# Performance work log

Measured on AMD Instinct MI355X. Metric: run time of the kernel, lower is better.

Reference implementation:

```python
import math
import jax, jax.numpy as jnp
import numpy as np

B, S, D, H, V, NZ = 2, 2048, 1024, 16, 4096, 10
DK = D // H
KAPPA = 1.0
GAMMA_VALS = [14.1347, 21.022, 25.0109, 30.4249, 32.9351,
              37.5862, 40.9187, 43.3271, 48.0052, 49.7738]


def setup_inputs() -> dict:
    key = jax.random.key(0)
    ks = jax.random.split(key, 12)
    w_scale = 1.0 / math.sqrt(D)
    x = jax.random.normal(ks[0], (B, S, D), dtype=jnp.float32)
    wq = jax.random.normal(ks[1], (D, D), dtype=jnp.float32) * w_scale
    wk = jax.random.normal(ks[2], (D, D), dtype=jnp.float32) * w_scale
    wv = jax.random.normal(ks[3], (D, D), dtype=jnp.float32) * w_scale
    wo = jax.random.normal(ks[4], (D, D), dtype=jnp.float32) * w_scale
    bq = jax.random.normal(ks[5], (D,), dtype=jnp.float32) * 0.01
    bk = jax.random.normal(ks[6], (D,), dtype=jnp.float32) * 0.01
    bv = jax.random.normal(ks[7], (D,), dtype=jnp.float32) * 0.01
    bo = jax.random.normal(ks[8], (D,), dtype=jnp.float32) * 0.01
    semantic_token_ids = jax.random.randint(ks[9], (B, S), 0, V)
    # constitutional charter mask: mostly-allowed boolean (stored as float buffer)
    omega_mask = (jax.random.uniform(ks[10], (V, V)) < 0.95).astype(jnp.float32)
    causal_mask = jnp.tril(jnp.ones((S, S), dtype=bool))
    gamma = jnp.asarray(GAMMA_VALS[:NZ], dtype=jnp.float32)
    return {
        "x": x, "wq": wq, "bq": bq, "wk": wk, "bk": bk,
        "wv": wv, "bv": bv, "wo": wo, "bo": bo,
        "omega_mask": omega_mask, "gamma": gamma,
        "semantic_token_ids": semantic_token_ids, "causal_mask": causal_mask,
    }


def _memory_kernel(seq_len, gamma):
    idx = jnp.arange(seq_len, dtype=jnp.float32)
    delta = jnp.abs(idx[:, None] - idx[None, :])            # [S, S]
    decay = jnp.exp(-KAPPA * delta)
    log_delta = jnp.log(delta + 1.0)
    cos_sum = jnp.sum(jnp.cos(gamma[:, None, None] * log_delta[None]), axis=0)
    return decay * cos_sum                                   # [S, S]


def reference(x, wq, bq, wk, bk, wv, bv, wo, bo,
              omega_mask, gamma, semantic_token_ids, causal_mask):
    batch, seq_len, _ = x.shape
    q = (x @ wq.T + bq).reshape(batch, seq_len, H, DK)
    k = (x @ wk.T + bk).reshape(batch, seq_len, H, DK)
    v = (x @ wv.T + bv).reshape(batch, seq_len, H, DK)
    scores = jnp.einsum('bihd,bjhd->bhij', q, k) / math.sqrt(DK)  # [B,H,S,S]
    M = _memory_kernel(seq_len, gamma)                            # [S,S]
    scores = scores * M[None, None]
    # seq_omega[b,i,j] = omega_mask[ids[b,i], ids[b,j]]
    ids = semantic_token_ids
    seq_omega = omega_mask[ids[:, :, None], ids[:, None, :]]      # [B,S,S]
    scores = jnp.where(seq_omega[:, None] == 0, -1e9, scores)
    scores = jnp.where(causal_mask[None, None], scores, -1e9)
    attn = jax.nn.softmax(scores, axis=-1)
    out = jnp.einsum('bhij,bjhd->bihd', attn, v).reshape(batch, seq_len, D)
    return out @ wo.T + bo
```

## Files before the change

### kernel.cpp

```cpp
#include <hip/hip_runtime.h>
#include <math.h>
#include <float.h>

#define B_ 2
#define S_ 2048
#define D_ 1024
#define H_ 16
#define V_ 4096
#define NZ_ 10
#define BS_ (B_ * S_)

typedef __attribute__((ext_vector_type(8))) __bf16 bf16x8;
typedef __attribute__((ext_vector_type(4))) float f32x4;

#define MFMA16(a, b, c) __builtin_amdgcn_mfma_f32_16x16x32_bf16((a), (b), (c), 0, 0, 0)

__device__ __forceinline__ unsigned short f2bf(float f) {
  unsigned u = __builtin_bit_cast(unsigned, f);
  u = (u + 0x7FFFu + ((u >> 16) & 1u)) >> 16;
  return (unsigned short)u;
}
__device__ __forceinline__ float bf2f(unsigned short h) {
  unsigned u = ((unsigned)h) << 16;
  return __builtin_bit_cast(float, u);
}

__global__ __launch_bounds__(256) void prep_kernel(
    const float* __restrict__ x,
    const float* __restrict__ wq, const float* __restrict__ wk,
    const float* __restrict__ wv, const float* __restrict__ wo,
    const float* __restrict__ omega, const float* __restrict__ gamma,
    unsigned short* __restrict__ xh, unsigned short* __restrict__ xl,
    unsigned short* __restrict__ wqh, unsigned short* __restrict__ wql,
    unsigned short* __restrict__ wkh, unsigned short* __restrict__ wkl,
    unsigned short* __restrict__ wvh, unsigned short* __restrict__ woh,
    unsigned long long* __restrict__ obit, float* __restrict__ mbg) {
  const int bid = blockIdx.x;
  const int t = threadIdx.x;
  if (bid < 4096) {
    int i = (bid * 256 + t) * 4;
    float4 v = *(const float4*)(x + i);
    ushort4 h;
    h.x = f2bf(v.x); h.y = f2bf(v.y); h.z = f2bf(v.z); h.w = f2bf(v.w);
    *(ushort4*)(xh + i) = h;
    ushort4 l;
    l.x = f2bf(v.x - bf2f(h.x));
    l.y = f2bf(v.y - bf2f(h.y));
    l.z = f2bf(v.z - bf2f(h.z));
    l.w = f2bf(v.w - bf2f(h.w));
    *(ushort4*)(xl + i) = l;
  } else if (bid < 8192) {
    int idx = ((bid - 4096) * 256 + t) * 4;
    int w = idx >> 20;
    int off = idx & ((1 << 20) - 1);
    const float* src; unsigned short* hi; unsigned short* lo;
    if (w == 0)      { src = wq; hi = wqh; lo = wql; }
    else if (w == 1) { src = wk; hi = wkh; lo = wkl; }
    else if (w == 2) { src = wv; hi = wvh; lo = nullptr; }
    else             { src = wo; hi = woh; lo = nullptr; }
    float4 v = *(const float4*)(src + off);
    ushort4 h;
    h.x = f2bf(v.x); h.y = f2bf(v.y); h.z = f2bf(v.z); h.w = f2bf(v.w);
    *(ushort4*)(hi + off) = h;
    if (lo) {
      ushort4 l;
      l.x = f2bf(v.x - bf2f(h.x));
      l.y = f2bf(v.y - bf2f(h.y));
      l.z = f2bf(v.z - bf2f(h.z));
      l.w = f2bf(v.w - bf2f(h.w));
      *(ushort4*)(lo + off) = l;
    }
  } else if (bid < 8192 + 65536) {
    int e = (bid - 8192) * 256 + t;
    bool ok = omega[e] != 0.f;
    unsigned long long mask = __ballot(ok);
    if ((t & 63) == 0) obit[e >> 6] = mask;
  } else {
    if (t < 64) {
      float delta = (float)t;
      float ld = logf(delta + 1.f);
      float cs = 0.f;
#pragma unroll
      for (int z = 0; z < NZ_; ++z) cs += cosf(gamma[z] * ld);
      mbg[t] = expf(-delta) * cs * 0.125f;
    }
  }
}

template <int NT>
__device__ __forceinline__ void stage_tiles(const unsigned short* const* gb,
                                            int wave, int lane, int K, int k0,
                                            unsigned short* dst) {
#pragma unroll
  for (int tile = 0; tile < NT; ++tile) {
#pragma unroll
    for (int half = 0; half < 2; ++half) {
      int c = wave + half * 4;
      int s = (c << 6) + lane;
      int row = s >> 2;
      int cq = (s & 3) ^ ((s >> 3) & 3);
      const unsigned short* g = gb[tile] + (size_t)row * K + k0 + (cq << 3);
      unsigned short* l = dst + tile * 4096 + (s << 3);
      __builtin_amdgcn_global_load_lds((const __attribute__((address_space(1))) void*)g,
                                       (__attribute__((address_space(3))) void*)l,
                                       16, 0, 0);
    }
  }
}

__device__ __forceinline__ void frag_loads(const unsigned short* tb, int base, int wsel,
                                           int m, int quad, bf16x8 (&f)[4]) {
#pragma unroll
  for (int i = 0; i < 4; ++i) {
    int r = wsel * 64 + i * 16 + m;
    f[i] = *(const bf16x8*)&tb[base + r * 32 + ((quad ^ ((r >> 1) & 3)) << 3)];
  }
}

__device__ __forceinline__ void qkv_compute(const unsigned short* tb, bool split,
                                            int wm, int wn, int m, int quad,
                                            f32x4 (&acc)[4][4]) {
  bf16x8 afh[4], bfh[4];
  frag_loads(tb, 0 * 4096, wm, m, quad, afh);
  frag_loads(tb, 1 * 4096, wn, m, quad, bfh);
  if (split) {
    bf16x8 afl[4], bfl[4];
    frag_loads(tb, 2 * 4096, wm, m, quad, afl);
    frag_loads(tb, 3 * 4096, wn, m, quad, bfl);
#pragma unroll
    for (int mt = 0; mt < 4; ++mt)
#pragma unroll
      for (int nt = 0; nt < 4; ++nt) {
        acc[mt][nt] = MFMA16(afh[mt], bfh[nt], acc[mt][nt]);
        acc[mt][nt] = MFMA16(afl[mt], bfh[nt], acc[mt][nt]);
        acc[mt][nt] = MFMA16(afh[mt], bfl[nt], acc[mt][nt]);
      }
  } else {
#pragma unroll
    for (int mt = 0; mt < 4; ++mt)
#pragma unroll
      for (int nt = 0; nt < 4; ++nt)
        acc[mt][nt] = MFMA16(afh[mt], bfh[nt], acc[mt][nt]);
  }
}

__global__ __launch_bounds__(256) void mfma_gemm_qkv(
    const unsigned short* __restrict__ xh, const unsigned short* __restrict__ xl,
    const unsigned short* __restrict__ wqh, const unsigned short* __restrict__ wql,
    const unsigned short* __restrict__ wkh, const unsigned short* __restrict__ wkl,
    const unsigned short* __restrict__ wvh,
    const float* __restrict__ bq, const float* __restrict__ bk,
    const float* __restrict__ bv,
    unsigned short* __restrict__ qoh, unsigned short* __restrict__ qol,
    unsigned short* __restrict__ koh, unsigned short* __restrict__ kol,
    unsigned short* __restrict__ voh) {
  __shared__ unsigned short tiles[2][4 * 4096];
  const int t = threadIdx.x;
  const int wave = t >> 6, lane = t & 63;
  const int which = blockIdx.x >> 3;
  const int n0 = (blockIdx.x & 7) * 128;
  const int i0 = blockIdx.y * 128;
  const int K = D_, N = D_;
  const int wm = wave >> 1, wn = wave & 1;
  const int m = lane & 15, quad = lane >> 4;

  const unsigned short* Wh = (which == 0) ? wqh : (which == 1) ? wkh : wvh;
  const unsigned short* Wl = (which == 0) ? wql : wkl;
  const float* bias = (which == 0) ? bq : (which == 1) ? bk : bv;
  unsigned short* Chi = (which == 0) ? qoh : (which == 1) ? koh : voh;
  unsigned short* Clo = (which == 0) ? qol : (which == 1) ? kol : nullptr;
  const bool split = (which < 2);

  const unsigned short* gb[4];
  gb[0] = xh + (size_t)i0 * K;
  gb[1] = Wh + (size_t)n0 * K;
  gb[2] = xl + (size_t)i0 * K;
  gb[3] = Wl + (size_t)n0 * K;

  f32x4 acc[4][4] = {};

  if (split) stage_tiles<4>(gb, wave, lane, K, 0, tiles[0]);
  else       stage_tiles<2>(gb, wave, lane, K, 0, tiles[0]);
  __syncthreads();

  for (int k0 = 0; k0 < K; k0 += 64) {
    if (split) stage_tiles<4>(gb, wave, lane, K, k0 + 32, tiles[1]);
    else       stage_tiles<2>(gb, wave, lane, K, k0 + 32, tiles[1]);
    qkv_compute(tiles[0], split, wm, wn, m, quad, acc);
    __syncthreads();
    if (k0 + 64 < K) {
      if (split) stage_tiles<4>(gb, wave, lane, K, k0 + 64, tiles[0]);
      else       stage_tiles<2>(gb, wave, lane, K, k0 + 64, tiles[0]);
    }
    qkv_compute(tiles[1], split, wm, wn, m, quad, acc);
    __syncthreads();
  }

  float bvv[4];
#pragma unroll
  for (int nt = 0; nt < 4; ++nt) bvv[nt] = bias[n0 + wn * 64 + nt * 16 + m];
#pragma unroll
  for (int mt = 0; mt < 4; ++mt) {
    int rbase = i0 + wm * 64 + mt * 16 + quad * 4;
#pragma unroll
    for (int nt = 0; nt < 4; ++nt) {
      int col = n0 + wn * 64 + nt * 16 + m;
#pragma unroll
      for (int r = 0; r < 4; ++r) {
        float val = acc[mt][nt][r] + bvv[nt];
        size_t idx = (size_t)(rbase + r) * N + col;
        unsigned short hv = f2bf(val);
        Chi[idx] = hv;
        if (Clo) Clo[idx] = f2bf(val - bf2f(hv));
      }
    }
  }
}

__global__ __launch_bounds__(256) void mfma_gemm_o(const unsigned short* __restrict__ Ah,
                                                   const unsigned short* __restrict__ Wh,
                                                   const float* __restrict__ bias,
                                                   float* __restrict__ C,
                                                   int M, int N, int K) {
  __shared__ unsigned short tiles[2][2 * 4096];
  const int t = threadIdx.x;
  const int wave = t >> 6, lane = t & 63;
  const int i0 = blockIdx.y * 128, n0 = blockIdx.x * 128;
  const int wm = wave >> 1, wn = wave & 1;
  const int m = lane & 15, quad = lane >> 4;

  const unsigned short* gb[2];
  gb[0] = Ah + (size_t)i0 * K;
  gb[1] = Wh + (size_t)n0 * K;

  f32x4 acc[4][4] = {};

  stage_tiles<2>(gb, wave, lane, K, 0, tiles[0]);
  __syncthreads();

  for (int k0 = 0; k0 < K; k0 += 64) {
    stage_tiles<2>(gb, wave, lane, K, k0 + 32, tiles[1]);
    qkv_compute(tiles[0], false, wm, wn, m, quad, acc);
    __syncthreads();
    if (k0 + 64 < K) stage_tiles<2>(gb, wave, lane, K, k0 + 64, tiles[0]);
    qkv_compute(tiles[1], false, wm, wn, m, quad, acc);
    __syncthreads();
  }

  float bvv[4];
#pragma unroll
  for (int nt = 0; nt < 4; ++nt) bvv[nt] = bias[n0 + wn * 64 + nt * 16 + m];
#pragma unroll
  for (int mt = 0; mt < 4; ++mt) {
    int rbase = i0 + wm * 64 + mt * 16 + quad * 4;
#pragma unroll
    for (int nt = 0; nt < 4; ++nt) {
      int col = n0 + wn * 64 + nt * 16 + m;
#pragma unroll
      for (int r = 0; r < 4; ++r)
        C[(size_t)(rbase + r) * N + col] = acc[mt][nt][r] + bvv[nt];
    }
  }
}

__global__ void ts8_kernel(const unsigned short* __restrict__ vh, float* __restrict__ ts8) {
  int idx = blockIdx.x * 256 + threadIdx.x;
  int d = idx % D_;
  int bg = idx / D_;
  int g = bg % 256;
  int b = bg / 256;
  const unsigned short* p = vh + (size_t)(b * S_ + g * 8) * D_ + d;
  float s = 0.f;
#pragma unroll
  for (int j = 0; j < 8; ++j) s += bf2f(p[(size_t)j * D_]);
  ts8[idx] = s;
}

__global__ __launch_bounds__(256) void tsp_kernel(const float* __restrict__ ts8,
                                                  float* __restrict__ tsp) {
  int b = blockIdx.x >> 2;
  int d = ((blockIdx.x & 3) << 8) + threadIdx.x;
  float s = 0.f;
  tsp[((size_t)b * 33 + 0) * D_ + d] = 0.f;
  for (int u = 0; u < 256; ++u) {
    s += ts8[((size_t)b * 256 + u) * D_ + d];
    if ((u & 7) == 7) tsp[((size_t)b * 33 + (u >> 3) + 1) * D_ + d] = s;
  }
}

__global__ __launch_bounds__(256) void farsum_kernel(const unsigned short* __restrict__ vh,
                                                     const float* __restrict__ ts8,
                                                     const float* __restrict__ tsp,
                                                     const int* __restrict__ ids,
                                                     const unsigned long long* __restrict__ obit,
                                                     unsigned short* __restrict__ farsum,
                                                     int* __restrict__ c0,
                                                     unsigned long long* __restrict__ bm) {
  const int b = blockIdx.x / S_;
  const int i = blockIdx.x % S_;
  const int t = threadIdx.x;
  const int idi = ids[b * S_ + i];
  const unsigned long long* orow = obit + ((size_t)idi << 6);

  if (t < 64) {
    int jj = i - t;
    bool ok = false;
    if (jj >= 0) {
      int idj = ids[b * S_ + jj];
      ok = (orow[idj >> 6] >> (idj & 63)) & 1ull;
    }
    unsigned long long mask = __ballot(ok);
    if (t == 0) bm[blockIdx.x] = mask;
  }

  if (i < 64) {
    if (t == 0) c0[blockIdx.x] = 0;
    return;
  }
  const int jmax = i - 64;
  const int F = jmax + 1;
  const int d0 = t * 4;
  const int T = F >> 6;
  const int G8 = (F & 63) >> 3;

  float4 acc = *(const float4*)(tsp + ((size_t)b * 33 + T) * D_ + d0);
  for (int u = 0; u < G8; ++u) {
    float4 x = *(const float4*)(ts8 + ((size_t)b * 256 + T * 8 + u) * D_ + d0);
    acc.x += x.x; acc.y += x.y; acc.z += x.z; acc.w += x.w;
  }
  for (int j = (T << 6) + (G8 << 3); j <= jmax; ++j) {
    ushort4 x = *(const ushort4*)(vh + ((size_t)(b * S_) + j) * D_ + d0);
    acc.x += bf2f(x.x); acc.y += bf2f(x.y);
    acc.z += bf2f(x.z); acc.w += bf2f(x.w);
  }

  __shared__ int list[256];
  __shared__ int cnt;
  int nmask = 0;
  for (int base = 0; base < F; base += 256) {
    if (t == 0) cnt = 0;
    __syncthreads();
    int j = base + t;
    if (j <= jmax) {
      int idj = ids[b * S_ + j];
      if (!((orow[idj >> 6] >> (idj & 63)) & 1ull)) list[atomicAdd(&cnt, 1)] = j;
    }
    __syncthreads();
    int c = cnt;
    nmask += c;
    for (int mm = 0; mm < c; ++mm) {
      int jm = list[mm];
      ushort4 x = *(const ushort4*)(vh + ((size_t)(b * S_) + jm) * D_ + d0);
      acc.x -= bf2f(x.x); acc.y -= bf2f(x.y);
      acc.z -= bf2f(x.z); acc.w -= bf2f(x.w);
    }
    __syncthreads();
  }
  ushort4 o;
  o.x = f2bf(acc.x); o.y = f2bf(acc.y); o.z = f2bf(acc.z); o.w = f2bf(acc.w);
  *(ushort4*)(farsum + (size_t)(b * S_ + i) * D_ + d0) = o;
  if (t == 0) c0[blockIdx.x] = F - nmask;
}

__global__ __launch_bounds__(256, 3) void attn4_kernel(
    const unsigned short* __restrict__ qh, const unsigned short* __restrict__ ql,
    const unsigned short* __restrict__ kh, const unsigned short* __restrict__ kl,
    const unsigned short* __restrict__ vh, const unsigned short* __restrict__ farsum,
    const int* __restrict__ c0arr, const float* __restrict__ tsp,
    const unsigned long long* __restrict__ bm, const float* __restrict__ mbg,
    unsigned short* __restrict__ out) {
  const int h = blockIdx.x, i0 = blockIdx.y * 64, b = blockIdx.z;
  const int jt0 = i0 - 64;
  __shared__ unsigned short Qhs[64 * 72];
  __shared__ unsigned short Khs[128 * 72];
  __shared__ unsigned short Vt[64 * 136];
  __shared__ float mrow[64], lrow[64], Mband[64];
  __shared__ float rmaxw[4][32], rsumw[4][32];
  __shared__ unsigned long long bmr[64];
  __shared__ int c0r[64];
  const int t = threadIdx.x, lane = t & 63, wave = t >> 6;
  const int m = lane & 15, quad = lane >> 4;
  const int wm = wave >> 1, wn = wave & 1;

  bf16x8 aL[2][2], bL[4][2];
#pragma unroll
  for (int mt = 0; mt < 2; ++mt)
#pragma unroll
    for (int kc = 0; kc < 2; ++kc) {
      int row = i0 + wm * 32 + mt * 16 + m;
      aL[mt][kc] = *(const bf16x8*)(ql + ((size_t)(b * S_) + row) * D_ + h * 64 + kc * 32 + quad * 8);
    }
#pragma unroll
  for (int nt = 0; nt < 4; ++nt)
#pragma unroll
    for (int kc = 0; kc < 2; ++kc) {
      int jr = jt0 + wn * 64 + nt * 16 + m;
      if (jr < 0) jr = 0;
      bL[nt][kc] = *(const bf16x8*)(kl + ((size_t)(b * S_) + jr) * D_ + h * 64 + kc * 32 + quad * 8);
    }

  for (int c = t; c < 1024; c += 256) {
    int r = c >> 4, d4 = (c & 15) << 2;
    size_t g = ((size_t)(b * S_) + i0 + r) * D_ + h * 64 + d4;
    *(ushort4*)&Qhs[r * 72 + d4] = *(const ushort4*)(qh + g);
  }
  for (int c = t; c < 2048; c += 256) {
    int r = c >> 4, d4 = (c & 15) << 2;
    int jr = jt0 + r;
    if (jr < 0) jr = 0;
    size_t g = ((size_t)(b * S_) + jr) * D_ + h * 64 + d4;
    *(ushort4*)&Khs[r * 72 + d4] = *(const ushort4*)(kh + g);
    ushort4 vv = *(const ushort4*)(vh + g);
    Vt[(d4 + 0) * 136 + r] = vv.x; Vt[(d4 + 1) * 136 + r] = vv.y;
    Vt[(d4 + 2) * 136 + r] = vv.z; Vt[(d4 + 3) * 136 + r] = vv.w;
  }
  if (t < 64) {
    Mband[t] = mbg[t];
    int grow = b * S_ + i0 + t;
    bmr[t] = bm[grow];
    int c0v = c0arr[grow];
    c0r[t] = c0v;
    mrow[t] = (c0v > 0) ? 0.f : -FLT_MAX;
  }
  __syncthreads();

  f32x4 accS[2][4] = {};
#pragma unroll
  for (int kc = 0; kc < 2; ++kc) {
    bf16x8 aH[2], bH[4];
#pragma unroll
    for (int mt = 0; mt < 2; ++mt)
      aH[mt] = *(const bf16x8*)&Qhs[(wm * 32 + mt * 16 + m) * 72 + kc * 32 + quad * 8];
#pragma unroll
    for (int nt = 0; nt < 4; ++nt)
      bH[nt] = *(const bf16x8*)&Khs[(wn * 64 + nt * 16 + m) * 72 + kc * 32 + quad * 8];
#pragma unroll
    for (int mt = 0; mt < 2; ++mt)
#pragma unroll
      for (int nt = 0; nt < 4; ++nt) {
        accS[mt][nt] = MFMA16(aH[mt], bH[nt], accS[mt][nt]);
        accS[mt][nt] = MFMA16(aL[mt][kc], bH[nt], accS[mt][nt]);
        accS[mt][nt] = MFMA16(aH[mt], bL[nt][kc], accS[mt][nt]);
      }
  }

  float rmx[2][4];
#pragma unroll
  for (int mt = 0; mt < 2; ++mt)
#pragma unroll
    for (int r = 0; r < 4; ++r) rmx[mt][r] = -FLT_MAX;
#pragma unroll
  for (int mt = 0; mt < 2; ++mt)
#pragma unroll
    for (int nt = 0; nt < 4; ++nt)
#pragma unroll
      for (int r = 0; r < 4; ++r) {
        int il = wm * 32 + mt * 16 + quad * 4 + r;
        int jl = wn * 64 + nt * 16 + m;
        int dlt = il + 64 - jl;
        float s = -FLT_MAX;
        if (dlt >= 0 && dlt < 64 && ((bmr[il] >> dlt) & 1ull))
          s = accS[mt][nt][r] * Mband[dlt];
        accS[mt][nt][r] = s;
        rmx[mt][r] = fmaxf(rmx[mt][r], s);
      }
#pragma unroll
  for (int off = 1; off < 16; off <<= 1)
#pragma unroll
    for (int mt = 0; mt < 2; ++mt)
#pragma unroll
      for (int r = 0; r < 4; ++r)
        rmx[mt][r] = fmaxf(rmx[mt][r], __shfl_xor(rmx[mt][r], off));
  if (m == 0)
#pragma unroll
    for (int mt = 0; mt < 2; ++mt)
#pragma unroll
      for (int r = 0; r < 4; ++r)
        rmaxw[wave][mt * 16 + quad * 4 + r] = rmx[mt][r];
  __syncthreads();
  if (t < 64) {
    int wmw = t >> 5, idx = t & 31;
    float tmax = fmaxf(rmaxw[wmw * 2][idx], rmaxw[wmw * 2 + 1][idx]);
    mrow[t] = fmaxf(mrow[t], tmax);
  }
  __syncthreads();

  unsigned short* Pl = Khs;
  float rs[2][4] = {};
#pragma unroll
  for (int mt = 0; mt < 2; ++mt)
#pragma unroll
    for (int nt = 0; nt < 4; ++nt)
#pragma unroll
      for (int r = 0; r < 4; ++r) {
        int il = wm * 32 + mt * 16 + quad * 4 + r;
        int jl = wn * 64 + nt * 16 + m;
        float s = accS[mt][nt][r];
        float p = (s > -1e37f) ? expf(s - mrow[il]) : 0.f;
        rs[mt][r] += p;
        Pl[il * 136 + jl] = f2bf(p);
      }
#pragma unroll
  for (int off = 1; off < 16; off <<= 1)
#pragma unroll
    for (int mt = 0; mt < 2; ++mt)
#pragma unroll
      for (int r = 0; r < 4; ++r)
        rs[mt][r] += __shfl_xor(rs[mt][r], off);
  if (m == 0)
#pragma unroll
    for (int mt = 0; mt < 2; ++mt)
#pragma unroll
      for (int r = 0; r < 4; ++r)
        rsumw[wave][mt * 16 + quad * 4 + r] = rs[mt][r];
  __syncthreads();
  if (t < 64) {
    int wmw = t >> 5, idx = t & 31;
    lrow[t] = rsumw[wmw * 2][idx] + rsumw[wmw * 2 + 1][idx];
  }

  f32x4 accO[2][2] = {};
#pragma unroll
  for (int kc = 0; kc < 4; ++kc) {
    bf16x8 aP[2], bV[2];
#pragma unroll
    for (int mt = 0; mt < 2; ++mt)
      aP[mt] = *(const bf16x8*)&Pl[(wm * 32 + mt * 16 + m) * 136 + kc * 32 + quad * 8];
#pragma unroll
    for (int nt = 0; nt < 2; ++nt)
      bV[nt] = *(const bf16x8*)&Vt[(wn * 32 + nt * 16 + m) * 136 + kc * 32 + quad * 8];
#pragma unroll
    for (int mt = 0; mt < 2; ++mt)
#pragma unroll
      for (int nt = 0; nt < 2; ++nt)
        accO[mt][nt] = MFMA16(aP[mt], bV[nt], accO[mt][nt]);
  }
  __syncthreads();

#pragma unroll
  for (int mt = 0; mt < 2; ++mt)
#pragma unroll
    for (int r = 0; r < 4; ++r) {
      int il = wm * 32 + mt * 16 + quad * 4 + r;
      int gi = i0 + il;
      float mv = mrow[il], l = lrow[il];
      int C0 = c0r[il];
      float efar = (C0 > 0) ? expf(-mv) : 0.f;
      float denom = l + (float)C0 * efar;
      bool degen = (l == 0.f && C0 == 0);
      if (degen) denom = (float)S_;
      float inv = 1.f / denom;
#pragma unroll
      for (int nt = 0; nt < 2; ++nt) {
        int d = wn * 32 + nt * 16 + m;
        size_t base = ((size_t)(b * S_) + gi) * D_ + h * 64 + d;
        float o = accO[mt][nt][r];
        if (C0 > 0) o += efar * bf2f(farsum[base]);
        if (degen) o = tsp[((size_t)b * 33 + 32) * D_ + h * 64 + d];
        out[base] = f2bf(o * inv);
      }
    }
}

extern "C" void kernel_launch(void* const* d_in, const int* in_sizes, int n_in,
                              void* d_out, int out_size, void* d_ws, size_t ws_size,
                              hipStream_t stream) {
  const float* x     = (const float*)d_in[0];
  const float* wq    = (const float*)d_in[1];
  const float* bq    = (const float*)d_in[2];
  const float* wk    = (const float*)d_in[3];
  const float* bk    = (const float*)d_in[4];
  const float* wv    = (const float*)d_in[5];
  const float* bv    = (const float*)d_in[6];
  const float* wo    = (const float*)d_in[7];
  const float* bo    = (const float*)d_in[8];
  const float* omega = (const float*)d_in[9];
  const float* gamma = (const float*)d_in[10];
  const int*   ids   = (const int*)d_in[11];
  float* out = (float*)d_out;

  char* ws = (char*)d_ws;
  const size_t SZH = (size_t)BS_ * D_ * 2;
  const size_t WH  = (size_t)D_ * D_ * 2;
  unsigned short* qhb = (unsigned short*)(ws);
  unsigned short* qlb = (unsigned short*)(ws + 1 * SZH);
  unsigned short* khb = (unsigned short*)(ws + 2 * SZH);
  unsigned short* klb = (unsigned short*)(ws + 3 * SZH);
  unsigned short* vhb = (unsigned short*)(ws + 4 * SZH);
  unsigned short* xl    = (unsigned short*)(ws + 5 * SZH);
  unsigned short* fsumh = xl;
  unsigned short* xh    = (unsigned short*)(ws + 6 * SZH);
  unsigned short* ah    = xh;
  char* wp = ws + 7 * SZH;
  unsigned short* wqh = (unsigned short*)(wp);
  unsigned short* wql = (unsigned short*)(wp + 1 * WH);
  unsigned short* wkh = (unsigned short*)(wp + 2 * WH);
  unsigned short* wkl = (unsigned short*)(wp + 3 * WH);
  unsigned short* wvh = (unsigned short*)(wp + 4 * WH);
  unsigned short* woh = (unsigned short*)(wp + 5 * WH);
  char* tail = wp + 6 * WH;
  unsigned long long* obit = (unsigned long long*)tail;
  float* ts8  = (float*)(tail + (size_t)V_ * 64 * 8);
  float* ts64 = (float*)((char*)ts8 + (size_t)B_ * 256 * D_ * 4);
  float* tsp  = (float*)((char*)ts64 + (size_t)B_ * 32 * D_ * 4);
  int* c0 = (int*)((char*)tsp + (size_t)B_ * 33 * D_ * 4);
  unsigned long long* bmask = (unsigned long long*)((char*)c0 + (size_t)BS_ * 4);
  float* mbg = (float*)((char*)bmask + (size_t)BS_ * 8);

  prep_kernel<<<8192 + 65536 + 1, 256, 0, stream>>>(
      x, wq, wk, wv, wo, omega, gamma,
      xh, xl, wqh, wql, wkh, wkl, wvh, woh, obit, mbg);

  mfma_gemm_qkv<<<dim3(24, 32), 256, 0, stream>>>(xh, xl, wqh, wql, wkh, wkl, wvh,
                                                  bq, bk, bv, qhb, qlb, khb, klb, vhb);

  ts8_kernel<<<(B_ * 256 * D_) / 256, 256, 0, stream>>>(vhb, ts8);
  tsp_kernel<<<B_ * 4, 256, 0, stream>>>(ts8, tsp);
  farsum_kernel<<<B_ * S_, 256, 0, stream>>>(vhb, ts8, tsp, ids, obit, fsumh, c0, bmask);
  attn4_kernel<<<dim3(H_, S_ / 64, B_), 256, 0, stream>>>(qhb, qlb, khb, klb, vhb, fsumh, c0,
                                                          tsp, bmask, mbg, ah);

  mfma_gemm_o<<<dim3(D_ / 128, BS_ / 128), 256, 0, stream>>>(ah, woh, bo, out, BS_, D_, D_);
}
```

Measured before the change: 400.4 us.

## Parallelize prefix sums and replace shared-list masking with per-wave ballot iteration

The serial tsp prefix kernel, which ran on only 8 blocks and looped 256 times per thread, is replaced by two wide kernels: one reduces groups of eight ts8 rows into ts64, and one computes each prefix entry directly. In farsum, the shared-memory list built with atomics and guarded by three barriers per 256-column chunk is replaced by a wave-level ballot over 64 columns, iterating set bits with ctz. This removes block syncs and LDS atomics, at the cost of an extra launch and some redundant prefix work. Each wave now walks its own masked bits, and the result is unchanged because every wave covers the full range.

Result: no change. 398.2 us (-0.5%).

```diff
diff --git a/kernel.cpp b/kernel.cpp
--- a/kernel.cpp
+++ b/kernel.cpp
@@ -276,16 +276,27 @@
   ts8[idx] = s;
 }
 
-__global__ __launch_bounds__(256) void tsp_kernel(const float* __restrict__ ts8,
-                                                  float* __restrict__ tsp) {
-  int b = blockIdx.x >> 2;
-  int d = ((blockIdx.x & 3) << 8) + threadIdx.x;
+__global__ void ts64_kernel(const float* __restrict__ ts8, float* __restrict__ ts64) {
+  int idx = blockIdx.x * 256 + threadIdx.x;
+  int d = idx % D_;
+  int bT = idx / D_;
+  int T = bT % 32;
+  int b = bT / 32;
   float s = 0.f;
-  tsp[((size_t)b * 33 + 0) * D_ + d] = 0.f;
-  for (int u = 0; u < 256; ++u) {
-    s += ts8[((size_t)b * 256 + u) * D_ + d];
-    if ((u & 7) == 7) tsp[((size_t)b * 33 + (u >> 3) + 1) * D_ + d] = s;
-  }
+#pragma unroll
+  for (int u = 0; u < 8; ++u) s += ts8[((size_t)b * 256 + T * 8 + u) * D_ + d];
+  ts64[idx] = s;
+}
+
+__global__ void tsp2_kernel(const float* __restrict__ ts64, float* __restrict__ tsp) {
+  int idx = blockIdx.x * 256 + threadIdx.x;
+  int d = idx % D_;
+  int bT = idx / D_;
+  int T = bT % 33;
+  int b = bT / 33;
+  float s = 0.f;
+  for (int u = 0; u < T; ++u) s += ts64[((size_t)b * 32 + u) * D_ + d];
+  tsp[idx] = s;
 }
 
 __global__ __launch_bounds__(256) void farsum_kernel(const unsigned short* __restrict__ vh,
@@ -299,6 +310,7 @@
   const int b = blockIdx.x / S_;
   const int i = blockIdx.x % S_;
   const int t = threadIdx.x;
+  const int lane = t & 63;
   const int idi = ids[b * S_ + i];
   const unsigned long long* orow = obit + ((size_t)idi << 6);
 
@@ -334,28 +346,26 @@
     acc.z += bf2f(x.z); acc.w += bf2f(x.w);
   }
 
-  __shared__ int list[256];
-  __shared__ int cnt;
   int nmask = 0;
-  for (int base = 0; base < F; base += 256) {
-    if (t == 0) cnt = 0;
-    __syncthreads();
-    int j = base + t;
+  for (int base = 0; base < F; base += 64) {
+    int j = base + lane;
+    bool masked = false;
     if (j <= jmax) {
       int idj = ids[b * S_ + j];
-      if (!((orow[idj >> 6] >> (idj & 63)) & 1ull)) list[atomicAdd(&cnt, 1)] = j;
-    }
-    __syncthreads();
-    int c = cnt;
-    nmask += c;
-    for (int mm = 0; mm < c; ++mm) {
-      int jm = list[mm];
+      masked = !((orow[idj >> 6] >> (idj & 63)) & 1ull);
+    }
+    unsigned long long mk = __ballot(masked);
+    nmask += (int)__popcll(mk);
+    while (mk) {
+      int p = (int)__builtin_ctzll(mk);
+      mk &= mk - 1;
+      int jm = base + p;
       ushort4 x = *(const ushort4*)(vh + ((size_t)(b * S_) + jm) * D_ + d0);
       acc.x -= bf2f(x.x); acc.y -= bf2f(x.y);
       acc.z -= bf2f(x.z); acc.w -= bf2f(x.w);
     }
-    __syncthreads();
-  }
+  }
+
   ushort4 o;
   o.x = f2bf(acc.x); o.y = f2bf(acc.y); o.z = f2bf(acc.z); o.w = f2bf(acc.w);
   *(ushort4*)(farsum + (size_t)(b * S_ + i) * D_ + d0) = o;
@@ -615,7 +625,8 @@
                                                   bq, bk, bv, qhb, qlb, khb, klb, vhb);
 
   ts8_kernel<<<(B_ * 256 * D_) / 256, 256, 0, stream>>>(vhb, ts8);
-  tsp_kernel<<<B_ * 4, 256, 0, stream>>>(ts8, tsp);
+  ts64_kernel<<<(B_ * 32 * D_) / 256, 256, 0, stream>>>(ts8, ts64);
+  tsp2_kernel<<<(B_ * 33 * D_) / 256, 256, 0, stream>>>(ts64, tsp);
   farsum_kernel<<<B_ * S_, 256, 0, stream>>>(vhb, ts8, tsp, ids, obit, fsumh, c0, bmask);
   attn4_kernel<<<dim3(H_, S_ / 64, B_), 256, 0, stream>>>(qhb, qlb, khb, klb, vhb, fsumh, c0,
                                                           tsp, bmask, mbg, ah);
```

## Compute far-field masked V sums as a bitmask MFMA GEMM over transposed V

Applied to the files above, without the earlier changes.

The far-field sum of allowed V rows is now computed as a GEMM between a 0/1 mask matrix, expanded from per-row bitmasks into bf16, and a transposed V stored as [B,D,S]. The old per-row prefix-sum-minus-masked-list loop is removed. A new maskbits kernel builds the bitmasks and counts, and the QKV GEMM writes V transposed through LDS. The attention kernel also stages the K low part in LDS and loads V from the transposed layout. Blocks in the triangular GEMM are paired long with short for balance, but the GEMM does more raw FLOPs than the sparse subtraction approach.

After: 361.2 us. 1.11x faster.

```diff
diff --git a/kernel.cpp b/kernel.cpp
--- a/kernel.cpp
+++ b/kernel.cpp
@@ -12,6 +12,7 @@
 
 typedef __attribute__((ext_vector_type(8))) __bf16 bf16x8;
 typedef __attribute__((ext_vector_type(4))) float f32x4;
+typedef unsigned long long ull;
 
 #define MFMA16(a, b, c) __builtin_amdgcn_mfma_f32_16x16x32_bf16((a), (b), (c), 0, 0, 0)
 
@@ -34,7 +35,7 @@
     unsigned short* __restrict__ wqh, unsigned short* __restrict__ wql,
     unsigned short* __restrict__ wkh, unsigned short* __restrict__ wkl,
     unsigned short* __restrict__ wvh, unsigned short* __restrict__ woh,
-    unsigned long long* __restrict__ obit, float* __restrict__ mbg) {
+    ull* __restrict__ obit, float* __restrict__ mbg) {
   const int bid = blockIdx.x;
   const int t = threadIdx.x;
   if (bid < 4096) {
@@ -73,7 +74,7 @@
   } else if (bid < 8192 + 65536) {
     int e = (bid - 8192) * 256 + t;
     bool ok = omega[e] != 0.f;
-    unsigned long long mask = __ballot(ok);
+    ull mask = __ballot(ok);
     if ((t & 63) == 0) obit[e >> 6] = mask;
   } else {
     if (t < 64) {
@@ -85,6 +86,50 @@
       mbg[t] = expf(-delta) * cs * 0.125f;
     }
   }
+}
+
+__global__ __launch_bounds__(256) void maskbits_kernel(const int* __restrict__ ids,
+                                                       const ull* __restrict__ obit,
+                                                       ull* __restrict__ fmask,
+                                                       int* __restrict__ c0,
+                                                       ull* __restrict__ bm) {
+  const int grow = blockIdx.x;
+  const int b = grow >> 11, i = grow & 2047;
+  const int t = threadIdx.x, lane = t & 63, wave = t >> 6;
+  const int idi = ids[grow];
+  const ull* orow = obit + ((size_t)idi << 6);
+  __shared__ int cnt;
+  if (t == 0) cnt = 0;
+  if (t < 64) {
+    int jj = i - t;
+    bool ok = false;
+    if (jj >= 0) {
+      int idj = ids[b * S_ + jj];
+      ok = (orow[idj >> 6] >> (idj & 63)) & 1ull;
+    }
+    ull mask = __ballot(ok);
+    if (t == 0) bm[grow] = mask;
+  }
+  __syncthreads();
+  const int jmax = i - 64;
+  int pc = 0;
+#pragma unroll
+  for (int c = 0; c < 8; ++c) {
+    int j = c * 256 + t;
+    bool on = false;
+    if (j <= jmax) {
+      int idj = ids[b * S_ + j];
+      on = (orow[idj >> 6] >> (idj & 63)) & 1ull;
+    }
+    ull mk = __ballot(on);
+    if (lane == 0) {
+      fmask[(size_t)grow * 32 + c * 4 + wave] = mk;
+      pc += (int)__popcll(mk);
+    }
+  }
+  if (lane == 0 && pc) atomicAdd(&cnt, pc);
+  __syncthreads();
+  if (t == 0) c0[grow] = cnt;
 }
 
 template <int NT>
@@ -153,7 +198,7 @@
     const float* __restrict__ bv,
     unsigned short* __restrict__ qoh, unsigned short* __restrict__ qol,
     unsigned short* __restrict__ koh, unsigned short* __restrict__ kol,
-    unsigned short* __restrict__ voh) {
+    unsigned short* __restrict__ vt) {
   __shared__ unsigned short tiles[2][4 * 4096];
   const int t = threadIdx.x;
   const int wave = t >> 6, lane = t & 63;
@@ -167,7 +212,7 @@
   const unsigned short* Wh = (which == 0) ? wqh : (which == 1) ? wkh : wvh;
   const unsigned short* Wl = (which == 0) ? wql : wkl;
   const float* bias = (which == 0) ? bq : (which == 1) ? bk : bv;
-  unsigned short* Chi = (which == 0) ? qoh : (which == 1) ? koh : voh;
+  unsigned short* Chi = (which == 0) ? qoh : (which == 1) ? koh : vt;
   unsigned short* Clo = (which == 0) ? qol : (which == 1) ? kol : nullptr;
   const bool split = (which < 2);
 
@@ -199,19 +244,46 @@
   float bvv[4];
 #pragma unroll
   for (int nt = 0; nt < 4; ++nt) bvv[nt] = bias[n0 + wn * 64 + nt * 16 + m];
-#pragma unroll
-  for (int mt = 0; mt < 4; ++mt) {
-    int rbase = i0 + wm * 64 + mt * 16 + quad * 4;
-#pragma unroll
-    for (int nt = 0; nt < 4; ++nt) {
-      int col = n0 + wn * 64 + nt * 16 + m;
-#pragma unroll
-      for (int r = 0; r < 4; ++r) {
-        float val = acc[mt][nt][r] + bvv[nt];
-        size_t idx = (size_t)(rbase + r) * N + col;
-        unsigned short hv = f2bf(val);
-        Chi[idx] = hv;
-        if (Clo) Clo[idx] = f2bf(val - bf2f(hv));
+
+  if (which == 2) {
+    unsigned short* E = &tiles[0][0];
+#pragma unroll
+    for (int mt = 0; mt < 4; ++mt)
+#pragma unroll
+      for (int nt = 0; nt < 4; ++nt) {
+        int lc = wn * 64 + nt * 16 + m;
+#pragma unroll
+        for (int r = 0; r < 4; ++r) {
+          int lr = wm * 64 + mt * 16 + quad * 4 + r;
+          E[lr * 132 + lc] = f2bf(acc[mt][nt][r] + bvv[nt]);
+        }
+      }
+    __syncthreads();
+    const int bq2 = i0 >> 11, il0 = i0 & 2047;
+    for (int c = t; c < 4096; c += 256) {
+      int lcol = c >> 5, i4 = (c & 31) << 2;
+      ushort4 vv;
+      vv.x = E[(i4 + 0) * 132 + lcol];
+      vv.y = E[(i4 + 1) * 132 + lcol];
+      vv.z = E[(i4 + 2) * 132 + lcol];
+      vv.w = E[(i4 + 3) * 132 + lcol];
+      *(ushort4*)(Chi + ((size_t)bq2 * D_ + n0 + lcol) * S_ + il0 + i4) = vv;
+    }
+  } else {
+#pragma unroll
+    for (int mt = 0; mt < 4; ++mt) {
+      int rbase = i0 + wm * 64 + mt * 16 + quad * 4;
+#pragma unroll
+      for (int nt = 0; nt < 4; ++nt) {
+        int col = n0 + wn * 64 + nt * 16 + m;
+#pragma unroll
+        for (int r = 0; r < 4; ++r) {
+          float val = acc[mt][nt][r] + bvv[nt];
+          size_t idx = (size_t)(rbase + r) * N + col;
+          unsigned short hv = f2bf(val);
+          Chi[idx] = hv;
+          Clo[idx] = f2bf(val - bf2f(hv));
+        }
       }
     }
   }
@@ -263,120 +335,152 @@
   }
 }
 
-__global__ void ts8_kernel(const unsigned short* __restrict__ vh, float* __restrict__ ts8) {
-  int idx = blockIdx.x * 256 + threadIdx.x;
-  int d = idx % D_;
-  int bg = idx / D_;
-  int g = bg % 256;
-  int b = bg / 256;
-  const unsigned short* p = vh + (size_t)(b * S_ + g * 8) * D_ + d;
+__global__ void ts8_kernel(const unsigned short* __restrict__ vt, float* __restrict__ ts8) {
+  int tid = blockIdx.x * 256 + threadIdx.x;
+  int g = tid & 255;
+  int dg = tid >> 8;
+  const unsigned short* p = vt + (size_t)dg * S_ + g * 8;
+  ushort4 a = *(const ushort4*)p;
+  ushort4 b4 = *(const ushort4*)(p + 4);
+  ts8[tid] = bf2f(a.x) + bf2f(a.y) + bf2f(a.z) + bf2f(a.w) +
+             bf2f(b4.x) + bf2f(b4.y) + bf2f(b4.z) + bf2f(b4.w);
+}
+
+__global__ void ts64_kernel(const float* __restrict__ ts8, float* __restrict__ ts64) {
+  int tid = blockIdx.x * 256 + threadIdx.x;
+  int T = tid & 31;
+  int dg = tid >> 5;
+  const float* p = ts8 + (size_t)dg * 256 + T * 8;
+  float4 x = *(const float4*)p;
+  float4 y = *(const float4*)(p + 4);
+  ts64[tid] = x.x + x.y + x.z + x.w + y.x + y.y + y.z + y.w;
+}
+
+__global__ void tsp2_kernel(const float* __restrict__ ts64, float* __restrict__ tsp) {
+  int tid = blockIdx.x * 256 + threadIdx.x;
+  int T = tid % 33;
+  int dg = tid / 33;
   float s = 0.f;
-#pragma unroll
-  for (int j = 0; j < 8; ++j) s += bf2f(p[(size_t)j * D_]);
-  ts8[idx] = s;
-}
-
-__global__ __launch_bounds__(256) void tsp_kernel(const float* __restrict__ ts8,
-                                                  float* __restrict__ tsp) {
-  int b = blockIdx.x >> 2;
-  int d = ((blockIdx.x & 3) << 8) + threadIdx.x;
-  float s = 0.f;
-  tsp[((size_t)b * 33 + 0) * D_ + d] = 0.f;
-  for (int u = 0; u < 256; ++u) {
-    s += ts8[((size_t)b * 256 + u) * D_ + d];
-    if ((u & 7) == 7) tsp[((size_t)b * 33 + (u >> 3) + 1) * D_ + d] = s;
-  }
-}
-
-__global__ __launch_bounds__(256) void farsum_kernel(const unsigned short* __restrict__ vh,
-                                                     const float* __restrict__ ts8,
-                                                     const float* __restrict__ tsp,
-                                                     const int* __restrict__ ids,
-                                                     const unsigned long long* __restrict__ obit,
-                                                     unsigned short* __restrict__ farsum,
-                                                     int* __restrict__ c0,
-                                                     unsigned long long* __restrict__ bm) {
-  const int b = blockIdx.x / S_;
-  const int i = blockIdx.x % S_;
-  const int t = threadIdx.x;
-  const int idi = ids[b * S_ + i];
-  const unsigned long long* orow = obit + ((size_t)idi << 6);
-
-  if (t < 64) {
-    int jj = i - t;
-    bool ok = false;
-    if (jj >= 0) {
-      int idj = ids[b * S_ + jj];
-      ok = (orow[idj >> 6] >> (idj & 63)) & 1ull;
-    }
-    unsigned long long mask = __ballot(ok);
-    if (t == 0) bm[blockIdx.x] = mask;
-  }
-
-  if (i < 64) {
-    if (t == 0) c0[blockIdx.x] = 0;
-    return;
-  }
-  const int jmax = i - 64;
-  const int F = jmax + 1;
-  const int d0 = t * 4;
-  const int T = F >> 6;
-  const int G8 = (F & 63) >> 3;
-
-  float4 acc = *(const float4*)(tsp + ((size_t)b * 33 + T) * D_ + d0);
-  for (int u = 0; u < G8; ++u) {
-    float4 x = *(const float4*)(ts8 + ((size_t)b * 256 + T * 8 + u) * D_ + d0);
-    acc.x += x.x; acc.y += x.y; acc.z += x.z; acc.w += x.w;
-  }
-  for (int j = (T << 6) + (G8 << 3); j <= jmax; ++j) {
-    ushort4 x = *(const ushort4*)(vh + ((size_t)(b * S_) + j) * D_ + d0);
-    acc.x += bf2f(x.x); acc.y += bf2f(x.y);
-    acc.z += bf2f(x.z); acc.w += bf2f(x.w);
-  }
-
-  __shared__ int list[256];
-  __shared__ int cnt;
-  int nmask = 0;
-  for (int base = 0; base < F; base += 256) {
-    if (t == 0) cnt = 0;
+  for (int u = 0; u < T; ++u) s += ts64[(size_t)dg * 32 + u];
+  tsp[tid] = s;
+}
+
+__device__ __forceinline__ void fs_buildA(const ull* __restrict__ fm0, int t, int k0,
+                                          unsigned short* dstA) {
+  int row = t >> 2, q = t & 3;
+  int cq = q ^ ((row >> 1) & 3);
+  int kb = k0 + (cq << 3);
+  ull w = fm0[(size_t)row * 32 + (kb >> 6)];
+  unsigned byte = (unsigned)(w >> (kb & 63)) & 0xFFu;
+  uint4 v;
+  v.x = ((byte & 1u)   ? 0x3F80u : 0u) | ((byte & 2u)   ? 0x3F800000u : 0u);
+  v.y = ((byte & 4u)   ? 0x3F80u : 0u) | ((byte & 8u)   ? 0x3F800000u : 0u);
+  v.z = ((byte & 16u)  ? 0x3F80u : 0u) | ((byte & 32u)  ? 0x3F800000u : 0u);
+  v.w = ((byte & 64u)  ? 0x3F80u : 0u) | ((byte & 128u) ? 0x3F800000u : 0u);
+  *(uint4*)&dstA[t << 3] = v;
+}
+
+__device__ __forceinline__ void fs_stageB(const unsigned short* __restrict__ Bb,
+                                          int wave, int lane, int k0,
+                                          unsigned short* dstB) {
+#pragma unroll
+  for (int half = 0; half < 2; ++half) {
+    int c = wave + half * 4;
+    int s = (c << 6) + lane;
+    int row = s >> 2;
+    int cq = (s & 3) ^ ((s >> 3) & 3);
+    const unsigned short* g = Bb + (size_t)row * S_ + k0 + (cq << 3);
+    __builtin_amdgcn_global_load_lds((const __attribute__((address_space(1))) void*)g,
+                                     (__attribute__((address_space(3))) void*)(dstB + (s << 3)),
+                                     16, 0, 0);
+  }
+}
+
+__device__ __forceinline__ void fs_compute(const unsigned short* tb,
+                                           int wm, int wn, int m, int quad,
+                                           f32x4 (&acc)[2][4]) {
+  bf16x8 af[2], bf[4];
+#pragma unroll
+  for (int i = 0; i < 2; ++i) {
+    int r = wm * 32 + i * 16 + m;
+    af[i] = *(const bf16x8*)&tb[r * 32 + ((quad ^ ((r >> 1) & 3)) << 3)];
+  }
+#pragma unroll
+  for (int i = 0; i < 4; ++i) {
+    int r = wn * 64 + i * 16 + m;
+    bf[i] = *(const bf16x8*)&tb[2048 + r * 32 + ((quad ^ ((r >> 1) & 3)) << 3)];
+  }
+#pragma unroll
+  for (int mt = 0; mt < 2; ++mt)
+#pragma unroll
+    for (int nt = 0; nt < 4; ++nt)
+      acc[mt][nt] = MFMA16(af[mt], bf[nt], acc[mt][nt]);
+}
+
+__global__ __launch_bounds__(256) void farsum_gemm(const unsigned short* __restrict__ vt,
+                                                   const ull* __restrict__ fmask,
+                                                   unsigned short* __restrict__ fsum) {
+  __shared__ unsigned short ft[2][6144];
+  const int t = threadIdx.x, wave = t >> 6, lane = t & 63;
+  const int m = lane & 15, quad = lane >> 4;
+  const int wm = wave >> 1, wn = wave & 1;
+  const int n0 = blockIdx.x * 128;
+  const int y = blockIdx.y, half = y >> 5, u = y & 31;
+  const int b = u & 1;
+  const int q = half ? (u >> 1) : (31 - (u >> 1));
+  const int il0 = q * 64;
+  const int grow0 = b * S_ + il0;
+  const unsigned short* Bb = vt + ((size_t)b * D_ + n0) * S_;
+  const ull* fm0 = fmask + (size_t)grow0 * 32;
+  const int kend = il0;
+
+  f32x4 acc[2][4] = {};
+  if (kend > 0) {
+    fs_stageB(Bb, wave, lane, 0, &ft[0][2048]);
+    fs_buildA(fm0, t, 0, &ft[0][0]);
     __syncthreads();
-    int j = base + t;
-    if (j <= jmax) {
-      int idj = ids[b * S_ + j];
-      if (!((orow[idj >> 6] >> (idj & 63)) & 1ull)) list[atomicAdd(&cnt, 1)] = j;
-    }
-    __syncthreads();
-    int c = cnt;
-    nmask += c;
-    for (int mm = 0; mm < c; ++mm) {
-      int jm = list[mm];
-      ushort4 x = *(const ushort4*)(vh + ((size_t)(b * S_) + jm) * D_ + d0);
-      acc.x -= bf2f(x.x); acc.y -= bf2f(x.y);
-      acc.z -= bf2f(x.z); acc.w -= bf2f(x.w);
-    }
-    __syncthreads();
-  }
-  ushort4 o;
-  o.x = f2bf(acc.x); o.y = f2bf(acc.y); o.z = f2bf(acc.z); o.w = f2bf(acc.w);
-  *(ushort4*)(farsum + (size_t)(b * S_ + i) * D_ + d0) = o;
-  if (t == 0) c0[blockIdx.x] = F - nmask;
+    for (int k0 = 0; k0 < kend; k0 += 64) {
+      fs_stageB(Bb, wave, lane, k0 + 32, &ft[1][2048]);
+      fs_buildA(fm0, t, k0 + 32, &ft[1][0]);
+      fs_compute(&ft[0][0], wm, wn, m, quad, acc);
+      __syncthreads();
+      if (k0 + 64 < kend) {
+        fs_stageB(Bb, wave, lane, k0 + 64, &ft[0][2048]);
+        fs_buildA(fm0, t, k0 + 64, &ft[0][0]);
+      }
+      fs_compute(&ft[1][0], wm, wn, m, quad, acc);
+      __syncthreads();
+    }
+  }
+#pragma unroll
+  for (int mt = 0; mt < 2; ++mt)
+#pragma unroll
+    for (int nt = 0; nt < 4; ++nt) {
+      int col = n0 + wn * 64 + nt * 16 + m;
+#pragma unroll
+      for (int r = 0; r < 4; ++r) {
+        int row = grow0 + wm * 32 + mt * 16 + quad * 4 + r;
+        fsum[(size_t)row * D_ + col] = f2bf(acc[mt][nt][r]);
+      }
+    }
 }
 
 __global__ __launch_bounds__(256, 3) void attn4_kernel(
     const unsigned short* __restrict__ qh, const unsigned short* __restrict__ ql,
     const unsigned short* __restrict__ kh, const unsigned short* __restrict__ kl,
-    const unsigned short* __restrict__ vh, const unsigned short* __restrict__ farsum,
+    const unsigned short* __restrict__ vt, const unsigned short* __restrict__ farsum,
     const int* __restrict__ c0arr, const float* __restrict__ tsp,
-    const unsigned long long* __restrict__ bm, const float* __restrict__ mbg,
+    const ull* __restrict__ bm, const float* __restrict__ mbg,
     unsigned short* __restrict__ out) {
   const int h = blockIdx.x, i0 = blockIdx.y * 64, b = blockIdx.z;
   const int jt0 = i0 - 64;
   __shared__ unsigned short Qhs[64 * 72];
   __shared__ unsigned short Khs[128 * 72];
+  __shared__ unsigned short KlP[128 * 72];
   __shared__ unsigned short Vt[64 * 136];
   __shared__ float mrow[64], lrow[64], Mband[64];
   __shared__ float rmaxw[4][32], rsumw[4][32];
-  __shared__ unsigned long long bmr[64];
+  __shared__ ull bmr[64];
   __shared__ int c0r[64];
   const int t = threadIdx.x, lane = t & 63, wave = t >> 6;
   const int m = lane & 15, quad = lane >> 4;
@@ -410,9 +514,14 @@
     if (jr < 0) jr = 0;
     size_t g = ((size_t)(b * S_) + jr) * D_ + h * 64 + d4;
     *(ushort4*)&Khs[r * 72 + d4] = *(const ushort4*)(kh + g);
-    ushort4 vv = *(const ushort4*)(vh + g);
-    Vt[(d4 + 0) * 136 + r] = vv.x; Vt[(d4 + 1) * 136 + r] = vv.y;
-    Vt[(d4 + 2) * 136 + r] = vv.z; Vt[(d4 + 3) * 136 + r] = vv.w;
+    *(ushort4*)&KlP[r * 72 + d4] = *(const ushort4*)(kl + g);
+  }
+  for (int c = t; c < 2048; c += 256) {
+    int d = c >> 5, j4 = (c & 31) << 2;
+    int j = jt0 + j4;
+    if (j < 0) j = 0;
+    *(ushort4*)&Vt[d * 136 + j4] =
+        *(const ushort4*)(vt + ((size_t)(b * D_) + h * 64 + d) * S_ + j);
   }
   if (t < 64) {
     Mband[t] = mbg[t];
@@ -440,7 +549,8 @@
       for (int nt = 0; nt < 4; ++nt) {
         accS[mt][nt] = MFMA16(aH[mt], bH[nt], accS[mt][nt]);
         accS[mt][nt] = MFMA16(aL[mt][kc], bH[nt], accS[mt][nt]);
-        accS[mt][nt] = MFMA16(aH[mt], bL[nt][kc], accS[mt][nt]);
+        bf16x8 bLo = *(const bf16x8*)&KlP[(wn * 64 + nt * 16 + m) * 72 + kc * 32 + quad * 8];
+        accS[mt][nt] = MFMA16(aH[mt], bLo, accS[mt][nt]);
       }
   }
 
@@ -556,7 +666,7 @@
         size_t base = ((size_t)(b * S_) + gi) * D_ + h * 64 + d;
         float o = accO[mt][nt][r];
         if (C0 > 0) o += efar * bf2f(farsum[base]);
-        if (degen) o = tsp[((size_t)b * 33 + 32) * D_ + h * 64 + d];
+        if (degen) o = tsp[(size_t)(b * D_ + h * 64 + d) * 33 + 32];
         out[base] = f2bf(o * inv);
       }
     }
@@ -586,7 +696,7 @@
   unsigned short* qlb = (unsigned short*)(ws + 1 * SZH);
   unsigned short* khb = (unsigned short*)(ws + 2 * SZH);
   unsigned short* klb = (unsigned short*)(ws + 3 * SZH);
-  unsigned short* vhb = (unsigned short*)(ws + 4 * SZH);
+  unsigned short* vtb = (unsigned short*)(ws + 4 * SZH);
   unsigned short* xl    = (unsigned short*)(ws + 5 * SZH);
   unsigned short* fsumh = xl;
   unsigned short* xh    = (unsigned short*)(ws + 6 * SZH);
@@ -599,25 +709,31 @@
   unsigned short* wvh = (unsigned short*)(wp + 4 * WH);
   unsigned short* woh = (unsigned short*)(wp + 5 * WH);
   char* tail = wp + 6 * WH;
-  unsigned long long* obit = (unsigned long long*)tail;
+  ull* obit = (ull*)tail;
   float* ts8  = (float*)(tail + (size_t)V_ * 64 * 8);
   float* ts64 = (float*)((char*)ts8 + (size_t)B_ * 256 * D_ * 4);
   float* tsp  = (float*)((char*)ts64 + (size_t)B_ * 32 * D_ * 4);
   int* c0 = (int*)((char*)tsp + (size_t)B_ * 33 * D_ * 4);
-  unsigned long long* bmask = (unsigned long long*)((char*)c0 + (size_t)BS_ * 4);
+  ull* bmask = (ull*)((char*)c0 + (size_t)BS_ * 4);
   float* mbg = (float*)((char*)bmask + (size_t)BS_ * 8);
+  ull* fmask = (ull*)((char*)mbg + 256);
 
   prep_kernel<<<8192 + 65536 + 1, 256, 0, stream>>>(
       x, wq, wk, wv, wo, omega, gamma,
       xh, xl, wqh, wql, wkh, wkl, wvh, woh, obit, mbg);
 
+  maskbits_kernel<<<BS_, 256, 0, stream>>>(ids, obit, fmask, c0, bmask);
+
   mfma_gemm_qkv<<<dim3(24, 32), 256, 0, stream>>>(xh, xl, wqh, wql, wkh, wkl, wvh,
-                                                  bq, bk, bv, qhb, qlb, khb, klb, vhb);
-
-  ts8_kernel<<<(B_ * 256 * D_) / 256, 256, 0, stream>>>(vhb, ts8);
-  tsp_kernel<<<B_ * 4, 256, 0, stream>>>(ts8, tsp);
-  farsum_kernel<<<B_ * S_, 256, 0, stream>>>(vhb, ts8, tsp, ids, obit, fsumh, c0, bmask);
-  attn4_kernel<<<dim3(H_, S_ / 64, B_), 256, 0, stream>>>(qhb, qlb, khb, klb, vhb, fsumh, c0,
+                                                  bq, bk, bv, qhb, qlb, khb, klb, vtb);
+
+  ts8_kernel<<<B_ * D_, 256, 0, stream>>>(vtb, ts8);
+  ts64_kernel<<<(B_ * D_ * 32) / 256, 256, 0, stream>>>(ts8, ts64);
+  tsp2_kernel<<<(B_ * D_ * 33) / 256, 256, 0, stream>>>(ts64, tsp);
+
+  farsum_gemm<<<dim3(D_ / 128, 64), 256, 0, stream>>>(vtb, fmask, fsumh);
+
+  attn4_kernel<<<dim3(H_, S_ / 64, B_), 256, 0, stream>>>(qhb, qlb, khb, klb, vtb, fsumh, c0,
                                                           tsp, bmask, mbg, ah);
 
   mfma_gemm_o<<<dim3(D_ / 128, BS_ / 128), 256, 0, stream>>>(ah, woh, bo, out, BS_, D_, D_);
```
